# Kernel optimization log

Measured on AMD Instinct MI355X. Metric: run time of the kernel, lower is better.

The kernel has to match this reference:

```python
import jax, jax.numpy as jnp
import numpy as np

N_NODES = 100_000
N_EDGES = 1_600_000
N_GRAPHS = 1_000
NODES_PER_GRAPH = 100
N_NODE_FEATS = 64
DIM_STATE = 32
DIM_OUT = 64
DIM_NODE_EMB = 64
HID = 128
HEADS = 8
BASES = 4


def _lin(key, out_f, in_f, bias=True):
    k1, k2 = jax.random.split(key)
    lim = 1.0 / np.sqrt(in_f)
    w = jax.random.uniform(k1, (out_f, in_f), minval=-lim, maxval=lim, dtype=jnp.float32)
    if not bias:
        return w
    b = jax.random.uniform(k2, (out_f,), minval=-lim, maxval=lim, dtype=jnp.float32)
    return w, b


def setup_inputs() -> dict:
    key = jax.random.key(0)
    ks = jax.random.split(key, 16)
    x = jax.random.normal(ks[0], (N_NODES, N_NODE_FEATS), dtype=jnp.float32)
    edge_index = jax.random.randint(ks[1], (2, N_EDGES), 0, N_NODES, dtype=jnp.int32)
    batch = jnp.arange(N_NODES, dtype=jnp.int32) // NODES_PER_GRAPH  # sorted segment ids
    n_atoms = jnp.full((N_GRAPHS, 1), NODES_PER_GRAPH, dtype=jnp.int32)  # consistent with batch
    z_e = jax.random.normal(ks[2], (N_GRAPHS, DIM_STATE), dtype=jnp.float32)
    nfc_w, nfc_b = _lin(ks[3], HID, N_NODE_FEATS)
    # EGConv: bases Linear(in, (out//heads)*bases, no bias); comb Linear(in, heads*bases); bias (out,)
    gc1_bases_w = _lin(ks[4], (HID // HEADS) * BASES, HID, bias=False)
    gc1_comb_w, gc1_comb_b = _lin(ks[5], HEADS * BASES, HID)
    gc1_bias = jnp.zeros((HID,), jnp.float32)
    gc2_bases_w = _lin(ks[6], (DIM_NODE_EMB // HEADS) * BASES, HID, bias=False)
    gc2_comb_w, gc2_comb_b = _lin(ks[7], HEADS * BASES, HID)
    gc2_bias = jnp.zeros((DIM_NODE_EMB,), jnp.float32)
    attn_w, attn_b = _lin(ks[8], 1, DIM_NODE_EMB + DIM_STATE)
    fcg_w, fcg_b = _lin(ks[9], DIM_OUT, DIM_NODE_EMB)
    fccg_w, fccg_b = _lin(ks[10], DIM_OUT, DIM_NODE_EMB)
    return {"x": x, "edge_index": edge_index, "batch": batch, "n_atoms": n_atoms, "z_e": z_e,
            "nfc_w": nfc_w, "nfc_b": nfc_b,
            "gc1_bases_w": gc1_bases_w, "gc1_comb_w": gc1_comb_w, "gc1_comb_b": gc1_comb_b, "gc1_bias": gc1_bias,
            "gc2_bases_w": gc2_bases_w, "gc2_comb_w": gc2_comb_w, "gc2_comb_b": gc2_comb_b, "gc2_bias": gc2_bias,
            "attn_w": attn_w, "attn_b": attn_b, "fcg_w": fcg_w, "fcg_b": fcg_b, "fccg_w": fccg_w, "fccg_b": fccg_b}


def _egconv(h, src, dst, bases_w, comb_w, comb_b, bias, heads=HEADS, nbases=BASES):
    # PyG EGConv with aggregators=['symnorm'], add_self_loops=True
    n = h.shape[0]
    out_ch = bias.shape[0]
    deg = jnp.ones((n,), h.dtype).at[dst].add(1.0)          # in-degree + self loop
    dis = jax.lax.rsqrt(deg)                                 # deg^-1/2
    b = h @ bases_w.T                                        # [n, nbases*(out_ch//heads)]
    # symnorm aggregation incl. self-loop term dis_i^2 * b_i
    agg = ((dis * dis)[:, None] * b).at[dst].add((dis[src] * dis[dst])[:, None] * b[src])
    w = (h @ comb_w.T + comb_b).reshape(n, heads, nbases)    # [n, H, B]
    agg = agg.reshape(n, nbases, out_ch // heads)            # [n, B, F/H]
    return jnp.einsum('nhb,nbf->nhf', w, agg).reshape(n, out_ch) + bias


def reference(x, edge_index, batch, n_atoms, z_e, nfc_w, nfc_b,
              gc1_bases_w, gc1_comb_w, gc1_comb_b, gc1_bias,
              gc2_bases_w, gc2_comb_w, gc2_comb_b, gc2_bias,
              attn_w, attn_b, fcg_w, fcg_b, fccg_w, fccg_b):
    src, dst = edge_index[0], edge_index[1]
    h = jax.nn.elu(x @ nfc_w.T + nfc_b)
    h = jax.nn.elu(_egconv(h, src, dst, gc1_bases_w, gc1_comb_w, gc1_comb_b, gc1_bias))
    h = jax.nn.elu(_egconv(h, src, dst, gc2_bases_w, gc2_comb_w, gc2_comb_b, gc2_bias))
    h = h / jnp.maximum(jnp.linalg.norm(h, axis=1, keepdims=True), 1e-12)  # L2 normalize
    z_a = jax.ops.segment_sum(h, batch, num_segments=N_GRAPHS) @ fcg_w.T + fcg_b
    z_rep = jnp.repeat(z_e, n_atoms[:, 0], axis=0, total_repeat_length=N_NODES)
    logits = jnp.concatenate([h, z_rep], axis=1) @ attn_w.T + attn_b + 1e-16  # [N,1]
    m = jax.ops.segment_max(logits, batch, num_segments=N_GRAPHS)
    e = jnp.exp(logits - m[batch])
    denom = jax.ops.segment_sum(e, batch, num_segments=N_GRAPHS) + 1e-16
    attns = e / denom[batch]
    z_c = jax.ops.segment_sum(attns * h, batch, num_segments=N_GRAPHS) @ fccg_w.T + fccg_b
    return z_a, z_c, h
```

## Files before the change

kernel.cpp:

```cpp
#include <hip/hip_runtime.h>
#include <hip/hip_bf16.h>
#include <math.h>

#define N_NODES  100000
#define N_EDGES  1600000
#define N_GRAPHS 1000
#define NPG      100
#define NBKT     391
#define BCAP     5120
#define EPB      4096
#define NBE      ((N_EDGES + EPB - 1) / EPB)

typedef float  f32x4 __attribute__((ext_vector_type(4)));
typedef short  s16x8 __attribute__((ext_vector_type(8)));

__device__ __forceinline__ float elu_f(float x) {
    return x > 0.0f ? x : expm1f(x);
}
__device__ __forceinline__ float bf2f(unsigned int u16) {
    union { unsigned int i; float f; } v; v.i = u16 << 16; return v.f;
}
__device__ __forceinline__ unsigned short f2bf(float f) {
    __hip_bfloat16 h = __float2bfloat16(f);
    return *reinterpret_cast<unsigned short*>(&h);
}
__device__ __forceinline__ s16x8 cvt8(const float4& a, const float4& b) {
    s16x8 o;
    o[0]=(short)f2bf(a.x); o[1]=(short)f2bf(a.y); o[2]=(short)f2bf(a.z); o[3]=(short)f2bf(a.w);
    o[4]=(short)f2bf(b.x); o[5]=(short)f2bf(b.y); o[6]=(short)f2bf(b.z); o[7]=(short)f2bf(b.w);
    return o;
}

__global__ __launch_bounds__(512) void init_cur_k(int* __restrict__ bkt_cur) {
    int t = threadIdx.x;
    if (t < NBKT) bkt_cur[t] = t * BCAP;
}

__global__ __launch_bounds__(256) void binscatter_k(
    const int* __restrict__ ei, int* __restrict__ bkt_cur, unsigned int* __restrict__ pairs,
    const float* __restrict__ w0, const float* __restrict__ w1c, const float* __restrict__ w1w,
    const float* __restrict__ w2c, const float* __restrict__ w2w, unsigned short* __restrict__ wb)
{
    if (blockIdx.x >= NBE) {
        int i = (int)(blockIdx.x - NBE) * 256 + threadIdx.x;
        float v;
        if (i < 8192)       v = w0[i];
        else if (i < 16384) v = w1c[i - 8192];
        else if (i < 20480) v = w1w[i - 16384];
        else if (i < 24576) v = w2c[i - 20480];
        else if (i < 28672) v = w2w[i - 24576];
        else return;
        wb[i] = f2bf(v);
        return;
    }

    __shared__ int h[NBKT];
    __shared__ int base[NBKT];
    const int t = threadIdx.x;
    for (int i = t; i < NBKT; i += 256) h[i] = 0;
    __syncthreads();
    const int4* src4 = (const int4*)ei;
    const int4* dst4 = (const int4*)(ei + N_EDGES);
    int i0 = blockIdx.x * (EPB / 4);
    for (int i = t; i < EPB / 4; i += 256) {
        int g = i0 + i;
        if (g < N_EDGES / 4) {
            int4 d = dst4[g];
            atomicAdd(&h[d.x >> 8], 1);
            atomicAdd(&h[d.y >> 8], 1);
            atomicAdd(&h[d.z >> 8], 1);
            atomicAdd(&h[d.w >> 8], 1);
        }
    }
    __syncthreads();
    for (int i = t; i < NBKT; i += 256) {
        int c = h[i];
        base[i] = c ? atomicAdd(&bkt_cur[i], c) : 0;
        h[i] = 0;
    }
    __syncthreads();
    for (int i = t; i < EPB / 4; i += 256) {
        int g = i0 + i;
        if (g < N_EDGES / 4) {
            int4 s4 = src4[g];
            int4 d4 = dst4[g];
            int b, r;
            b = d4.x >> 8; r = atomicAdd(&h[b], 1); pairs[base[b] + r] = ((unsigned)s4.x << 8) | (d4.x & 255);
            b = d4.y >> 8; r = atomicAdd(&h[b], 1); pairs[base[b] + r] = ((unsigned)s4.y << 8) | (d4.y & 255);
            b = d4.z >> 8; r = atomicAdd(&h[b], 1); pairs[base[b] + r] = ((unsigned)s4.z << 8) | (d4.z & 255);
            b = d4.w >> 8; r = atomicAdd(&h[b], 1); pairs[base[b] + r] = ((unsigned)s4.w << 8) | (d4.w & 255);
        }
    }
}

__global__ __launch_bounds__(256) void bucket_csr_k(const unsigned int* __restrict__ pairs,
                                                    const int* __restrict__ bkt_cur,
                                                    int* __restrict__ starts,
                                                    int* __restrict__ cnt,
                                                    float* __restrict__ dis,
                                                    int* __restrict__ srclist)
{
    __shared__ int s[256];
    __shared__ int cur[256];
    const int b = blockIdx.x, t = threadIdx.x;
    const int lo = b * BCAP;
    const int hi = bkt_cur[b];
    const int n0 = b << 8;
    const int nn = min(256, N_NODES - n0);

    s[t] = 0;
    __syncthreads();
    for (int i = lo + t; i < hi; i += 256) {
        unsigned int p = pairs[i];
        atomicAdd(&s[p & 255], 1);
    }
    __syncthreads();
    int v = s[t];
    __syncthreads();
    s[t] = v;
    __syncthreads();
    #pragma unroll
    for (int off = 1; off < 256; off <<= 1) {
        int u = (t >= off) ? s[t - off] : 0;
        __syncthreads();
        s[t] += u;
        __syncthreads();
    }
    int ex = lo + s[t] - v;
    if (t < nn) {
        starts[n0 + t] = ex;
        cnt[n0 + t] = v;
        dis[n0 + t] = rsqrtf(1.0f + (float)v);
    }
    cur[t] = ex;
    __syncthreads();
    for (int i = lo + t; i < hi; i += 256) {
        unsigned int p = pairs[i];
        int pos = atomicAdd(&cur[p & 255], 1);
        srclist[pos] = (int)(p >> 8);
    }
}

__global__ __launch_bounds__(256) void fusedA_k(
    const float* __restrict__ x, const unsigned short* __restrict__ wb,
    const float* __restrict__ b0, const float* __restrict__ bw,
    const float* __restrict__ dis, unsigned short* __restrict__ c1out,
    float* __restrict__ w1out, int M)
{
    __shared__ unsigned short hT[64][136];
    const unsigned short* W0b = wb;
    const unsigned short* Wcb = wb + 8192;
    const unsigned short* Wwb = wb + 16384;

    const int t = threadIdx.x;
    const int wave = t >> 6, lane = t & 63;
    const int lr = lane & 15, lk = lane >> 4;
    const int blockRow = blockIdx.x * 64;

    {
        const int wr = wave >> 1, wc = wave & 1;
        f32x4 acc[2][4];
        #pragma unroll
        for (int rt = 0; rt < 2; ++rt)
            #pragma unroll
            for (int ct = 0; ct < 4; ++ct) acc[rt][ct] = (f32x4){0.f,0.f,0.f,0.f};

        #pragma unroll
        for (int kt = 0; kt < 2; ++kt) {
            const int k0 = kt * 32 + lk * 8;
            s16x8 afr[2];
            #pragma unroll
            for (int rt = 0; rt < 2; ++rt) {
                int r = blockRow + (wr * 2 + rt) * 16 + lr;
                r = (r < M) ? r : (M - 1);
                const float* ap = x + (size_t)r * 64 + k0;
                afr[rt] = cvt8(*(const float4*)ap, *(const float4*)(ap + 4));
            }
            s16x8 bfr[4];
            #pragma unroll
            for (int ct = 0; ct < 4; ++ct) {
                int n = (wc * 4 + ct) * 16 + lr;
                bfr[ct] = *(const s16x8*)(W0b + (size_t)n * 64 + k0);
            }
            #pragma unroll
            for (int rt = 0; rt < 2; ++rt)
                #pragma unroll
                for (int ct = 0; ct < 4; ++ct)
                    acc[rt][ct] = __builtin_amdgcn_mfma_f32_16x16x32_bf16(afr[rt], bfr[ct], acc[rt][ct], 0, 0, 0);
        }
        #pragma unroll
        for (int rt = 0; rt < 2; ++rt) {
            int lmb = (wr * 2 + rt) * 16 + lk * 4;
            #pragma unroll
            for (int j = 0; j < 4; ++j) {
                #pragma unroll
                for (int ct = 0; ct < 4; ++ct) {
                    int n = (wc * 4 + ct) * 16 + lr;
                    hT[lmb + j][n] = f2bf(elu_f(acc[rt][ct][j] + b0[n]));
                }
            }
        }
    }
    __syncthreads();

    {
        f32x4 acc[6];
        #pragma unroll
        for (int ct = 0; ct < 6; ++ct) acc[ct] = (f32x4){0.f,0.f,0.f,0.f};
        #pragma unroll
        for (int kt = 0; kt < 4; ++kt) {
            const int k0 = kt * 32 + lk * 8;
            s16x8 af = *(const s16x8*)&hT[wave * 16 + lr][k0];
            #pragma unroll
            for (int ct = 0; ct < 6; ++ct) {
                int n = ct * 16 + lr;
                const unsigned short* wp = (n < 64) ? (Wcb + (size_t)n * 128 + k0)
                                                    : (Wwb + (size_t)(n - 64) * 128 + k0);
                acc[ct] = __builtin_amdgcn_mfma_f32_16x16x32_bf16(af, *(const s16x8*)wp, acc[ct], 0, 0, 0);
            }
        }
        int mbase = blockRow + wave * 16 + lk * 4;
        #pragma unroll
        for (int j = 0; j < 4; ++j) {
            int m = mbase + j;
            if (m >= M) continue;
            float dsc = dis[m];
            #pragma unroll
            for (int ct = 0; ct < 6; ++ct) {
                int n = ct * 16 + lr;
                float v = acc[ct][j];
                if (n < 64) c1out[(size_t)m * 64 + n] = f2bf(dsc * v);
                else        w1out[(size_t)m * 32 + (n - 64)] = v + bw[n - 64];
            }
        }
    }
}

__global__ __launch_bounds__(256) void mgemmL2_k(
    const unsigned short* __restrict__ Ab, const unsigned short* __restrict__ wb,
    const float* __restrict__ bw, const float* __restrict__ dis,
    unsigned short* __restrict__ c2out, float* __restrict__ w2out, int M)
{
    const unsigned short* Wcb = wb + 20480;
    const unsigned short* Wwb = wb + 24576;

    const int t = threadIdx.x;
    const int wave = t >> 6, lane = t & 63;
    const int wr = wave >> 1, wc = wave & 1;
    const int lr = lane & 15, lk = lane >> 4;
    const int blockRow = blockIdx.x * 64;

    f32x4 acc[2][2];
    #pragma unroll
    for (int rt = 0; rt < 2; ++rt)
        #pragma unroll
        for (int ct = 0; ct < 2; ++ct) acc[rt][ct] = (f32x4){0.f,0.f,0.f,0.f};

    #pragma unroll
    for (int kt = 0; kt < 4; ++kt) {
        const int k0 = kt * 32 + lk * 8;
        s16x8 afr[2];
        #pragma unroll
        for (int rt = 0; rt < 2; ++rt) {
            int r = blockRow + (wr * 2 + rt) * 16 + lr;
            r = (r < M) ? r : (M - 1);
            afr[rt] = *(const s16x8*)(Ab + (size_t)r * 128 + k0);
        }
        s16x8 bfr[2];
        #pragma unroll
        for (int ct = 0; ct < 2; ++ct) {
            int n = (wc * 2 + ct) * 16 + lr;
            const unsigned short* wp = (n < 32) ? (Wcb + (size_t)n * 128 + k0)
                                                : (Wwb + (size_t)(n - 32) * 128 + k0);
            bfr[ct] = *(const s16x8*)wp;
        }
        #pragma unroll
        for (int rt = 0; rt < 2; ++rt)
            #pragma unroll
            for (int ct = 0; ct < 2; ++ct)
                acc[rt][ct] = __builtin_amdgcn_mfma_f32_16x16x32_bf16(afr[rt], bfr[ct], acc[rt][ct], 0, 0, 0);
    }

    #pragma unroll
    for (int rt = 0; rt < 2; ++rt) {
        int mbase = blockRow + (wr * 2 + rt) * 16 + lk * 4;
        #pragma unroll
        for (int j = 0; j < 4; ++j) {
            int m = mbase + j;
            if (m >= M) continue;
            float dsc = dis[m];
            #pragma unroll
            for (int ct = 0; ct < 2; ++ct) {
                int n = (wc * 2 + ct) * 16 + lr;
                float v = acc[rt][ct][j];
                if (n < 32) c2out[(size_t)m * 32 + n] = f2bf(dsc * v);
                else        w2out[(size_t)m * 32 + (n - 32)] = v + bw[n - 32];
            }
        }
    }
}

__global__ __launch_bounds__(256) void gather1_k(
    const int* __restrict__ starts, const int* __restrict__ cnt,
    const int* __restrict__ srclist, const unsigned short* __restrict__ c,
    const float* __restrict__ w1, const float* __restrict__ dis,
    const float* __restrict__ bias, unsigned short* __restrict__ h2b)
{
    __shared__ float aggS[4][68];

    const int t = threadIdx.x;
    const int nn   = t >> 6;
    const int lane = t & 63;
    const int q    = lane & 15;
    const int slot = lane >> 4;
    const int n    = blockIdx.x * 4 + nn;

    const int s0 = starts[n];
    const int cn = cnt[n];
    float a0 = 0.f, a1 = 0.f, a2 = 0.f, a3 = 0.f;
    if (slot == 0) {
        uint2 u = *(const uint2*)(c + (size_t)n * 64 + q * 4);
        a0 = bf2f(u.x & 0xffff); a1 = bf2f(u.x >> 16);
        a2 = bf2f(u.y & 0xffff); a3 = bf2f(u.y >> 16);
    }
    for (int j = slot; j < cn; j += 4) {
        int src = srclist[s0 + j];
        uint2 u = *(const uint2*)(c + (size_t)src * 64 + q * 4);
        a0 += bf2f(u.x & 0xffff); a1 += bf2f(u.x >> 16);
        a2 += bf2f(u.y & 0xffff); a3 += bf2f(u.y >> 16);
    }
    a0 += __shfl_xor(a0, 16, 64); a0 += __shfl_xor(a0, 32, 64);
    a1 += __shfl_xor(a1, 16, 64); a1 += __shfl_xor(a1, 32, 64);
    a2 += __shfl_xor(a2, 16, 64); a2 += __shfl_xor(a2, 32, 64);
    a3 += __shfl_xor(a3, 16, 64); a3 += __shfl_xor(a3, 32, 64);
    if (slot == 0) {
        aggS[nn][q * 4 + 0] = a0;
        aggS[nn][q * 4 + 1] = a1;
        aggS[nn][q * 4 + 2] = a2;
        aggS[nn][q * 4 + 3] = a3;
    }
    __syncthreads();

    const float dn = dis[n];
    const float* wr = w1 + (size_t)n * 32;
    unsigned short* out = h2b + (size_t)n * 128;
    #pragma unroll
    for (int r = 0; r < 2; ++r) {
        int j = r * 64 + lane;
        int hh = j >> 4, f = j & 15;
        float4 wv = *(const float4*)(wr + hh * 4);
        float s = wv.x * aggS[nn][0 * 16 + f] + wv.y * aggS[nn][1 * 16 + f]
                + wv.z * aggS[nn][2 * 16 + f] + wv.w * aggS[nn][3 * 16 + f];
        out[j] = f2bf(elu_f(s * dn + bias[j]));
    }
}

__global__ __launch_bounds__(256) void gather2_k(
    const int* __restrict__ starts, const int* __restrict__ cnt,
    const int* __restrict__ srclist, const unsigned short* __restrict__ c,
    const float* __restrict__ w2, const float* __restrict__ dis,
    const float* __restrict__ bias, float* __restrict__ hout)
{
    __shared__ float aggS[4][36];

    const int t = threadIdx.x;
    const int nn   = t >> 6;
    const int lane = t & 63;
    const int q    = lane & 15;
    const int slot = lane >> 4;
    const int n    = blockIdx.x * 4 + nn;

    const int s0 = starts[n];
    const int cn = cnt[n];
    float a0 = 0.f, a1 = 0.f;
    if (slot == 0) {
        unsigned int u = *(const unsigned int*)(c + (size_t)n * 32 + q * 2);
        a0 = bf2f(u & 0xffff); a1 = bf2f(u >> 16);
    }
    for (int j = slot; j < cn; j += 4) {
        int src = srclist[s0 + j];
        unsigned int u = *(const unsigned int*)(c + (size_t)src * 32 + q * 2);
        a0 += bf2f(u & 0xffff); a1 += bf2f(u >> 16);
    }
    a0 += __shfl_xor(a0, 16, 64); a0 += __shfl_xor(a0, 32, 64);
    a1 += __shfl_xor(a1, 16, 64); a1 += __shfl_xor(a1, 32, 64);
    if (slot == 0) {
        aggS[nn][q * 2 + 0] = a0;
        aggS[nn][q * 2 + 1] = a1;
    }
    __syncthreads();

    const float dn = dis[n];
    const int hh = lane >> 3, f = lane & 7;
    float4 wv = *(const float4*)(w2 + (size_t)n * 32 + hh * 4);
    float s = wv.x * aggS[nn][0 * 8 + f] + wv.y * aggS[nn][1 * 8 + f]
            + wv.z * aggS[nn][2 * 8 + f] + wv.w * aggS[nn][3 * 8 + f];
    float sv = elu_f(s * dn + bias[lane]);

    float tot = sv * sv;
    #pragma unroll
    for (int o = 1; o < 64; o <<= 1) tot += __shfl_xor(tot, o, 64);
    float inv = 1.0f / fmaxf(sqrtf(tot), 1e-12f);
    hout[(size_t)n * 64 + lane] = sv * inv;
}

__global__ __launch_bounds__(128) void graph_k(const float* __restrict__ h,
                                               const float* __restrict__ z_e,
                                               const float* __restrict__ aw,
                                               const float* __restrict__ ab,
                                               const float* __restrict__ fcgw,
                                               const float* __restrict__ fcgb,
                                               const float* __restrict__ fccgw,
                                               const float* __restrict__ fccgb,
                                               float* __restrict__ z_a,
                                               float* __restrict__ z_c)
{
    __shared__ float Hs[NPG * 64];
    __shared__ float sumh[64], wsh[64], lg[NPG], ex[NPG];
    __shared__ float red[2];
    int g = blockIdx.x, t = threadIdx.x;
    const float* hg = h + (size_t)g * NPG * 64;
    for (int idx = t; idx < NPG * 64; idx += 128) Hs[idx] = hg[idx];
    __syncthreads();

    if (t < 64) {
        float s = 0.0f;
        for (int n = 0; n < NPG; ++n) s += Hs[n * 64 + t];
        sumh[t] = s;
    }
    __syncthreads();

    if (t < 64) {
        float acc = fcgb[t];
        for (int f = 0; f < 64; ++f) acc = fmaf(sumh[f], fcgw[t * 64 + f], acc);
        z_a[(size_t)g * 64 + t] = acc;
    }
    if (t < NPG) {
        float zd = 0.0f;
        for (int q = 0; q < 32; ++q) zd = fmaf(z_e[(size_t)g * 32 + q], aw[64 + q], zd);
        float dot = 0.0f;
        for (int k0 = 0; k0 < 64; ++k0) {
            int k = (k0 + t) & 63;
            dot = fmaf(Hs[t * 64 + k], aw[k], dot);
        }
        lg[t] = dot + zd + ab[0] + 1e-16f;
    }
    __syncthreads();

    if (t < 64) {
        float m = -INFINITY;
        for (int n = t; n < NPG; n += 64) m = fmaxf(m, lg[n]);
        #pragma unroll
        for (int o = 1; o < 64; o <<= 1) m = fmaxf(m, __shfl_xor(m, o, 64));
        if (t == 0) red[0] = m;
    }
    __syncthreads();
    float m = red[0];
    if (t < NPG) ex[t] = expf(lg[t] - m);
    __syncthreads();
    if (t < 64) {
        float s = 0.0f;
        for (int n = t; n < NPG; n += 64) s += ex[n];
        #pragma unroll
        for (int o = 1; o < 64; o <<= 1) s += __shfl_xor(s, o, 64);
        if (t == 0) red[1] = s + 1e-16f;
    }
    __syncthreads();
    float inv_denom = 1.0f / red[1];
    if (t < 64) {
        float a = 0.0f;
        for (int n = 0; n < NPG; ++n) a = fmaf(ex[n], Hs[n * 64 + t], a);
        wsh[t] = a * inv_denom;
    }
    __syncthreads();
    if (t < 64) {
        float acc = fccgb[t];
        for (int f = 0; f < 64; ++f) acc = fmaf(wsh[f], fccgw[t * 64 + f], acc);
        z_c[(size_t)g * 64 + t] = acc;
    }
}

extern "C" void kernel_launch(void* const* d_in, const int* in_sizes, int n_in,
                              void* d_out, int out_size, void* d_ws, size_t ws_size,
                              hipStream_t stream)
{
    const float* x     = (const float*)d_in[0];
    const int*   ei    = (const int*)d_in[1];
    const float* z_e   = (const float*)d_in[4];
    const float* nfc_w = (const float*)d_in[5];
    const float* nfc_b = (const float*)d_in[6];
    const float* g1bw  = (const float*)d_in[7];
    const float* g1cw  = (const float*)d_in[8];
    const float* g1cb  = (const float*)d_in[9];
    const float* g1b   = (const float*)d_in[10];
    const float* g2bw  = (const float*)d_in[11];
    const float* g2cw  = (const float*)d_in[12];
    const float* g2cb  = (const float*)d_in[13];
    const float* g2b   = (const float*)d_in[14];
    const float* aw    = (const float*)d_in[15];
    const float* ab    = (const float*)d_in[16];
    const float* fcgw  = (const float*)d_in[17];
    const float* fcgb  = (const float*)d_in[18];
    const float* fccgw = (const float*)d_in[19];
    const float* fccgb = (const float*)d_in[20];

    float* ws        = (float*)d_ws;
    float* dis       = ws;
    int*   cnt       = (int*)(ws + 102400);
    int*   starts    = cnt + 102400;
    int*   bkt_cur   = starts + 102400;
    int*   srclist   = bkt_cur + 512;
    float* hbuf      = (float*)(srclist + 2002048);
    float* c1f       = hbuf + 6400000;
    float* w1        = c1f + 3200000;
    float* c2f       = w1 + 3200000;
    float* w2        = c2f + 1600000;
    unsigned short* wb = (unsigned short*)(w2 + 3200000);
    unsigned int*  pairs = (unsigned int*)hbuf;
    unsigned short* hb = (unsigned short*)hbuf;
    unsigned short* c1 = (unsigned short*)c1f;
    unsigned short* c2 = (unsigned short*)c2f;

    float* z_a  = (float*)d_out;
    float* z_c  = z_a + (size_t)N_GRAPHS * 64;
    float* hout = z_a + (size_t)2 * N_GRAPHS * 64;

    const int GB = (N_NODES + 63) / 64;

    init_cur_k<<<1, 512, 0, stream>>>(bkt_cur);
    binscatter_k<<<NBE + 112, 256, 0, stream>>>(ei, bkt_cur, pairs,
                                                nfc_w, g1bw, g1cw, g2bw, g2cw, wb);
    bucket_csr_k<<<NBKT, 256, 0, stream>>>(pairs, bkt_cur, starts, cnt, dis, srclist);

    fusedA_k<<<GB, 256, 0, stream>>>(x, wb, nfc_b, g1cb, dis, c1, w1, N_NODES);
    gather1_k<<<N_NODES / 4, 256, 0, stream>>>(starts, cnt, srclist, c1, w1, dis, g1b, hb);
    mgemmL2_k<<<GB, 256, 0, stream>>>(hb, wb, g2cb, dis, c2, w2, N_NODES);
    gather2_k<<<N_NODES / 4, 256, 0, stream>>>(starts, cnt, srclist, c2, w2, dis, g2b, hout);
    graph_k<<<N_GRAPHS, 128, 0, stream>>>(hout, z_e, aw, ab, fcgw, fcgb, fccgw, fccgb, z_a, z_c);
}
```

Baseline: 249.4 us.

## Overlap edge bucketing with first GEMM by moving degree scaling into gather

The first dense GEMM no longer depends on node degrees because the dis[src] scaling moves from the GEMM epilogue into the layer-1 gather loop. That lets the edge bin-scatter blocks and the GEMM blocks share one launch, so the two independent workloads run concurrently. The weight conversion and bucket cursor init are merged into a single setup kernel, removing one launch. In exchange, the gather now loads dis[src] per edge, an extra random 4-byte read, and the scaling happens in fp32 after bf16 rounding rather than before.

New measurement: 239.9 us. 1.04x faster.

```diff
diff --git a/kernel.cpp b/kernel.cpp
--- a/kernel.cpp
+++ b/kernel.cpp
@@ -10,6 +10,7 @@
 #define BCAP     5120
 #define EPB      4096
 #define NBE      ((N_EDGES + EPB - 1) / EPB)
+#define GBA      ((N_NODES + 63) / 64)
 
 typedef float  f32x4 __attribute__((ext_vector_type(4)));
 typedef short  s16x8 __attribute__((ext_vector_type(8)));
@@ -31,64 +32,160 @@
     return o;
 }
 
-__global__ __launch_bounds__(512) void init_cur_k(int* __restrict__ bkt_cur) {
-    int t = threadIdx.x;
-    if (t < NBKT) bkt_cur[t] = t * BCAP;
-}
-
-__global__ __launch_bounds__(256) void binscatter_k(
-    const int* __restrict__ ei, int* __restrict__ bkt_cur, unsigned int* __restrict__ pairs,
+__global__ __launch_bounds__(512) void setup_k(
+    int* __restrict__ bkt_cur,
     const float* __restrict__ w0, const float* __restrict__ w1c, const float* __restrict__ w1w,
     const float* __restrict__ w2c, const float* __restrict__ w2w, unsigned short* __restrict__ wb)
 {
-    if (blockIdx.x >= NBE) {
-        int i = (int)(blockIdx.x - NBE) * 256 + threadIdx.x;
-        float v;
-        if (i < 8192)       v = w0[i];
-        else if (i < 16384) v = w1c[i - 8192];
-        else if (i < 20480) v = w1w[i - 16384];
-        else if (i < 24576) v = w2c[i - 20480];
-        else if (i < 28672) v = w2w[i - 24576];
-        else return;
-        wb[i] = f2bf(v);
+    int t = threadIdx.x;
+    if (blockIdx.x == 0 && t < NBKT) bkt_cur[t] = t * BCAP;
+    int i = blockIdx.x * 512 + t;
+    float v;
+    if (i < 8192)       v = w0[i];
+    else if (i < 16384) v = w1c[i - 8192];
+    else if (i < 20480) v = w1w[i - 16384];
+    else if (i < 24576) v = w2c[i - 20480];
+    else if (i < 28672) v = w2w[i - 24576];
+    else return;
+    wb[i] = f2bf(v);
+}
+
+__global__ __launch_bounds__(256) void scatterA_k(
+    const float* __restrict__ x, const unsigned short* __restrict__ wb,
+    const float* __restrict__ b0, const float* __restrict__ bw,
+    unsigned short* __restrict__ c1out, float* __restrict__ w1out, int M,
+    const int* __restrict__ ei, int* __restrict__ bkt_cur, unsigned int* __restrict__ pairs)
+{
+    __shared__ union {
+        struct { int h[NBKT]; int base[NBKT]; } sc;
+        unsigned short hT[64][136];
+    } u;
+
+    const int t = threadIdx.x;
+
+    if (blockIdx.x >= GBA) {
+        const int eb = blockIdx.x - GBA;
+        int* h = u.sc.h;
+        int* base = u.sc.base;
+        for (int i = t; i < NBKT; i += 256) h[i] = 0;
+        __syncthreads();
+        const int4* src4 = (const int4*)ei;
+        const int4* dst4 = (const int4*)(ei + N_EDGES);
+        int i0 = eb * (EPB / 4);
+        for (int i = t; i < EPB / 4; i += 256) {
+            int g = i0 + i;
+            if (g < N_EDGES / 4) {
+                int4 d = dst4[g];
+                atomicAdd(&h[d.x >> 8], 1);
+                atomicAdd(&h[d.y >> 8], 1);
+                atomicAdd(&h[d.z >> 8], 1);
+                atomicAdd(&h[d.w >> 8], 1);
+            }
+        }
+        __syncthreads();
+        for (int i = t; i < NBKT; i += 256) {
+            int c = h[i];
+            base[i] = c ? atomicAdd(&bkt_cur[i], c) : 0;
+            h[i] = 0;
+        }
+        __syncthreads();
+        for (int i = t; i < EPB / 4; i += 256) {
+            int g = i0 + i;
+            if (g < N_EDGES / 4) {
+                int4 s4 = src4[g];
+                int4 d4 = dst4[g];
+                int b, r;
+                b = d4.x >> 8; r = atomicAdd(&h[b], 1); pairs[base[b] + r] = ((unsigned)s4.x << 8) | (d4.x & 255);
+                b = d4.y >> 8; r = atomicAdd(&h[b], 1); pairs[base[b] + r] = ((unsigned)s4.y << 8) | (d4.y & 255);
+                b = d4.z >> 8; r = atomicAdd(&h[b], 1); pairs[base[b] + r] = ((unsigned)s4.z << 8) | (d4.z & 255);
+                b = d4.w >> 8; r = atomicAdd(&h[b], 1); pairs[base[b] + r] = ((unsigned)s4.w << 8) | (d4.w & 255);
+            }
+        }
         return;
     }
 
-    __shared__ int h[NBKT];
-    __shared__ int base[NBKT];
-    const int t = threadIdx.x;
-    for (int i = t; i < NBKT; i += 256) h[i] = 0;
-    __syncthreads();
-    const int4* src4 = (const int4*)ei;
-    const int4* dst4 = (const int4*)(ei + N_EDGES);
-    int i0 = blockIdx.x * (EPB / 4);
-    for (int i = t; i < EPB / 4; i += 256) {
-        int g = i0 + i;
-        if (g < N_EDGES / 4) {
-            int4 d = dst4[g];
-            atomicAdd(&h[d.x >> 8], 1);
-            atomicAdd(&h[d.y >> 8], 1);
-            atomicAdd(&h[d.z >> 8], 1);
-            atomicAdd(&h[d.w >> 8], 1);
-        }
-    }
-    __syncthreads();
-    for (int i = t; i < NBKT; i += 256) {
-        int c = h[i];
-        base[i] = c ? atomicAdd(&bkt_cur[i], c) : 0;
-        h[i] = 0;
-    }
-    __syncthreads();
-    for (int i = t; i < EPB / 4; i += 256) {
-        int g = i0 + i;
-        if (g < N_EDGES / 4) {
-            int4 s4 = src4[g];
-            int4 d4 = dst4[g];
-            int b, r;
-            b = d4.x >> 8; r = atomicAdd(&h[b], 1); pairs[base[b] + r] = ((unsigned)s4.x << 8) | (d4.x & 255);
-            b = d4.y >> 8; r = atomicAdd(&h[b], 1); pairs[base[b] + r] = ((unsigned)s4.y << 8) | (d4.y & 255);
-            b = d4.z >> 8; r = atomicAdd(&h[b], 1); pairs[base[b] + r] = ((unsigned)s4.z << 8) | (d4.z & 255);
-            b = d4.w >> 8; r = atomicAdd(&h[b], 1); pairs[base[b] + r] = ((unsigned)s4.w << 8) | (d4.w & 255);
+    const unsigned short* W0b = wb;
+    const unsigned short* Wcb = wb + 8192;
+    const unsigned short* Wwb = wb + 16384;
+
+    const int wave = t >> 6, lane = t & 63;
+    const int lr = lane & 15, lk = lane >> 4;
+    const int blockRow = blockIdx.x * 64;
+
+    {
+        const int wr = wave >> 1, wc = wave & 1;
+        f32x4 acc[2][4];
+        #pragma unroll
+        for (int rt = 0; rt < 2; ++rt)
+            #pragma unroll
+            for (int ct = 0; ct < 4; ++ct) acc[rt][ct] = (f32x4){0.f,0.f,0.f,0.f};
+
+        #pragma unroll
+        for (int kt = 0; kt < 2; ++kt) {
+            const int k0 = kt * 32 + lk * 8;
+            s16x8 afr[2];
+            #pragma unroll
+            for (int rt = 0; rt < 2; ++rt) {
+                int r = blockRow + (wr * 2 + rt) * 16 + lr;
+                r = (r < M) ? r : (M - 1);
+                const float* ap = x + (size_t)r * 64 + k0;
+                afr[rt] = cvt8(*(const float4*)ap, *(const float4*)(ap + 4));
+            }
+            s16x8 bfr[4];
+            #pragma unroll
+            for (int ct = 0; ct < 4; ++ct) {
+                int n = (wc * 4 + ct) * 16 + lr;
+                bfr[ct] = *(const s16x8*)(W0b + (size_t)n * 64 + k0);
+            }
+            #pragma unroll
+            for (int rt = 0; rt < 2; ++rt)
+                #pragma unroll
+                for (int ct = 0; ct < 4; ++ct)
+                    acc[rt][ct] = __builtin_amdgcn_mfma_f32_16x16x32_bf16(afr[rt], bfr[ct], acc[rt][ct], 0, 0, 0);
+        }
+        #pragma unroll
+        for (int rt = 0; rt < 2; ++rt) {
+            int lmb = (wr * 2 + rt) * 16 + lk * 4;
+            #pragma unroll
+            for (int j = 0; j < 4; ++j) {
+                #pragma unroll
+                for (int ct = 0; ct < 4; ++ct) {
+                    int n = (wc * 4 + ct) * 16 + lr;
+                    u.hT[lmb + j][n] = f2bf(elu_f(acc[rt][ct][j] + b0[n]));
+                }
+            }
+        }
+    }
+    __syncthreads();
+
+    {
+        f32x4 acc[6];
+        #pragma unroll
+        for (int ct = 0; ct < 6; ++ct) acc[ct] = (f32x4){0.f,0.f,0.f,0.f};
+        #pragma unroll
+        for (int kt = 0; kt < 4; ++kt) {
+            const int k0 = kt * 32 + lk * 8;
+            s16x8 af = *(const s16x8*)&u.hT[wave * 16 + lr][k0];
+            #pragma unroll
+            for (int ct = 0; ct < 6; ++ct) {
+                int n = ct * 16 + lr;
+                const unsigned short* wp = (n < 64) ? (Wcb + (size_t)n * 128 + k0)
+                                                    : (Wwb + (size_t)(n - 64) * 128 + k0);
+                acc[ct] = __builtin_amdgcn_mfma_f32_16x16x32_bf16(af, *(const s16x8*)wp, acc[ct], 0, 0, 0);
+            }
+        }
+        int mbase = blockRow + wave * 16 + lk * 4;
+        #pragma unroll
+        for (int j = 0; j < 4; ++j) {
+            int m = mbase + j;
+            if (m >= M) continue;
+            #pragma unroll
+            for (int ct = 0; ct < 6; ++ct) {
+                int n = ct * 16 + lr;
+                float v = acc[ct][j];
+                if (n < 64) c1out[(size_t)m * 64 + n] = f2bf(v);
+                else        w1out[(size_t)m * 32 + (n - 64)] = v + bw[n - 64];
+            }
         }
     }
 }
@@ -141,101 +238,6 @@
     }
 }
 
-__global__ __launch_bounds__(256) void fusedA_k(
-    const float* __restrict__ x, const unsigned short* __restrict__ wb,
-    const float* __restrict__ b0, const float* __restrict__ bw,
-    const float* __restrict__ dis, unsigned short* __restrict__ c1out,
-    float* __restrict__ w1out, int M)
-{
-    __shared__ unsigned short hT[64][136];
-    const unsigned short* W0b = wb;
-    const unsigned short* Wcb = wb + 8192;
-    const unsigned short* Wwb = wb + 16384;
-
-    const int t = threadIdx.x;
-    const int wave = t >> 6, lane = t & 63;
-    const int lr = lane & 15, lk = lane >> 4;
-    const int blockRow = blockIdx.x * 64;
-
-    {
-        const int wr = wave >> 1, wc = wave & 1;
-        f32x4 acc[2][4];
-        #pragma unroll
-        for (int rt = 0; rt < 2; ++rt)
-            #pragma unroll
-            for (int ct = 0; ct < 4; ++ct) acc[rt][ct] = (f32x4){0.f,0.f,0.f,0.f};
-
-        #pragma unroll
-        for (int kt = 0; kt < 2; ++kt) {
-            const int k0 = kt * 32 + lk * 8;
-            s16x8 afr[2];
-            #pragma unroll
-            for (int rt = 0; rt < 2; ++rt) {
-                int r = blockRow + (wr * 2 + rt) * 16 + lr;
-                r = (r < M) ? r : (M - 1);
-                const float* ap = x + (size_t)r * 64 + k0;
-                afr[rt] = cvt8(*(const float4*)ap, *(const float4*)(ap + 4));
-            }
-            s16x8 bfr[4];
-            #pragma unroll
-            for (int ct = 0; ct < 4; ++ct) {
-                int n = (wc * 4 + ct) * 16 + lr;
-                bfr[ct] = *(const s16x8*)(W0b + (size_t)n * 64 + k0);
-            }
-            #pragma unroll
-            for (int rt = 0; rt < 2; ++rt)
-                #pragma unroll
-                for (int ct = 0; ct < 4; ++ct)
-                    acc[rt][ct] = __builtin_amdgcn_mfma_f32_16x16x32_bf16(afr[rt], bfr[ct], acc[rt][ct], 0, 0, 0);
-        }
-        #pragma unroll
-        for (int rt = 0; rt < 2; ++rt) {
-            int lmb = (wr * 2 + rt) * 16 + lk * 4;
-            #pragma unroll
-            for (int j = 0; j < 4; ++j) {
-                #pragma unroll
-                for (int ct = 0; ct < 4; ++ct) {
-                    int n = (wc * 4 + ct) * 16 + lr;
-                    hT[lmb + j][n] = f2bf(elu_f(acc[rt][ct][j] + b0[n]));
-                }
-            }
-        }
-    }
-    __syncthreads();
-
-    {
-        f32x4 acc[6];
-        #pragma unroll
-        for (int ct = 0; ct < 6; ++ct) acc[ct] = (f32x4){0.f,0.f,0.f,0.f};
-        #pragma unroll
-        for (int kt = 0; kt < 4; ++kt) {
-            const int k0 = kt * 32 + lk * 8;
-            s16x8 af = *(const s16x8*)&hT[wave * 16 + lr][k0];
-            #pragma unroll
-            for (int ct = 0; ct < 6; ++ct) {
-                int n = ct * 16 + lr;
-                const unsigned short* wp = (n < 64) ? (Wcb + (size_t)n * 128 + k0)
-                                                    : (Wwb + (size_t)(n - 64) * 128 + k0);
-                acc[ct] = __builtin_amdgcn_mfma_f32_16x16x32_bf16(af, *(const s16x8*)wp, acc[ct], 0, 0, 0);
-            }
-        }
-        int mbase = blockRow + wave * 16 + lk * 4;
-        #pragma unroll
-        for (int j = 0; j < 4; ++j) {
-            int m = mbase + j;
-            if (m >= M) continue;
-            float dsc = dis[m];
-            #pragma unroll
-            for (int ct = 0; ct < 6; ++ct) {
-                int n = ct * 16 + lr;
-                float v = acc[ct][j];
-                if (n < 64) c1out[(size_t)m * 64 + n] = f2bf(dsc * v);
-                else        w1out[(size_t)m * 32 + (n - 64)] = v + bw[n - 64];
-            }
-        }
-    }
-}
-
 __global__ __launch_bounds__(256) void mgemmL2_k(
     const unsigned short* __restrict__ Ab, const unsigned short* __restrict__ wb,
     const float* __restrict__ bw, const float* __restrict__ dis,
@@ -319,15 +321,17 @@
     const int cn = cnt[n];
     float a0 = 0.f, a1 = 0.f, a2 = 0.f, a3 = 0.f;
     if (slot == 0) {
+        float dsn = dis[n];
         uint2 u = *(const uint2*)(c + (size_t)n * 64 + q * 4);
-        a0 = bf2f(u.x & 0xffff); a1 = bf2f(u.x >> 16);
-        a2 = bf2f(u.y & 0xffff); a3 = bf2f(u.y >> 16);
+        a0 = dsn * bf2f(u.x & 0xffff); a1 = dsn * bf2f(u.x >> 16);
+        a2 = dsn * bf2f(u.y & 0xffff); a3 = dsn * bf2f(u.y >> 16);
     }
     for (int j = slot; j < cn; j += 4) {
         int src = srclist[s0 + j];
+        float ds = dis[src];
         uint2 u = *(const uint2*)(c + (size_t)src * 64 + q * 4);
-        a0 += bf2f(u.x & 0xffff); a1 += bf2f(u.x >> 16);
-        a2 += bf2f(u.y & 0xffff); a3 += bf2f(u.y >> 16);
+        a0 = fmaf(ds, bf2f(u.x & 0xffff), a0); a1 = fmaf(ds, bf2f(u.x >> 16), a1);
+        a2 = fmaf(ds, bf2f(u.y & 0xffff), a2); a3 = fmaf(ds, bf2f(u.y >> 16), a3);
     }
     a0 += __shfl_xor(a0, 16, 64); a0 += __shfl_xor(a0, 32, 64);
     a1 += __shfl_xor(a1, 16, 64); a1 += __shfl_xor(a1, 32, 64);
@@ -525,16 +529,12 @@
     float* z_c  = z_a + (size_t)N_GRAPHS * 64;
     float* hout = z_a + (size_t)2 * N_GRAPHS * 64;
 
-    const int GB = (N_NODES + 63) / 64;
-
-    init_cur_k<<<1, 512, 0, stream>>>(bkt_cur);
-    binscatter_k<<<NBE + 112, 256, 0, stream>>>(ei, bkt_cur, pairs,
-                                                nfc_w, g1bw, g1cw, g2bw, g2cw, wb);
+    setup_k<<<57, 512, 0, stream>>>(bkt_cur, nfc_w, g1bw, g1cw, g2bw, g2cw, wb);
+    scatterA_k<<<GBA + NBE, 256, 0, stream>>>(x, wb, nfc_b, g1cb, c1, w1, N_NODES,
+                                              ei, bkt_cur, pairs);
     bucket_csr_k<<<NBKT, 256, 0, stream>>>(pairs, bkt_cur, starts, cnt, dis, srclist);
-
-    fusedA_k<<<GB, 256, 0, stream>>>(x, wb, nfc_b, g1cb, dis, c1, w1, N_NODES);
     gather1_k<<<N_NODES / 4, 256, 0, stream>>>(starts, cnt, srclist, c1, w1, dis, g1b, hb);
-    mgemmL2_k<<<GB, 256, 0, stream>>>(hb, wb, g2cb, dis, c2, w2, N_NODES);
+    mgemmL2_k<<<GBA, 256, 0, stream>>>(hb, wb, g2cb, dis, c2, w2, N_NODES);
     gather2_k<<<N_NODES / 4, 256, 0, stream>>>(starts, cnt, srclist, c2, w2, dis, g2b, hout);
     graph_k<<<N_GRAPHS, 128, 0, stream>>>(hout, z_e, aw, ab, fcgw, fcgb, fccgw, fccgb, z_a, z_c);
 }
```
